# Optimization experiments

Measured on AMD Instinct MI355X. Metric: run time of the kernel, lower is better.

The kernel has to match this reference:

```python
import jax, jax.numpy as jnp
import numpy as np

B, N, BS, H, DH, L, FF, V, R = 1, 4096, 64, 12, 64, 4, 3072, 30522, 3
D = H * DH
M = N // BS
NEG = -10000.0


def layernorm(x, g, b, eps=1e-5):
    mu = x.mean(-1, keepdims=True)
    var = ((x - mu) ** 2).mean(-1, keepdims=True)
    return (x - mu) * jax.lax.rsqrt(var + eps) * g + b


def bigbird_attention(q, k, v, band_mask, from_mask, to_mask, blocked_mask, rand_attn):
    # q,k,v: [b,h,n,d]; band_mask [b,1,m-4,BS,3BS]; to_mask [b,1,1,n]; from_mask [b,1,n,1]
    b, h, n, d = q.shape
    m = n // BS
    r = rand_attn.shape[-1]
    sc = 1.0 / jnp.sqrt(jnp.float32(d))
    qb = q.reshape(b, h, m, BS, d)
    kb = k.reshape(b, h, m, BS, d)
    vb = v.reshape(b, h, m, BS, d)
    hid = jnp.arange(h)[:, None, None]
    gk = kb[:, hid, rand_attn].reshape(b, h, m - 2, r * BS, d)  # gathered random keys
    gv = vb[:, hid, rand_attn].reshape(b, h, m - 2, r * BS, d)
    rand_to = blocked_mask[:, rand_attn].reshape(b, h, m - 2, r * BS)
    rand_mask = jnp.einsum('blq,bhlk->bhlqk', blocked_mask[:, 1:-1], rand_to)  # [b,h,m-2,BS,rBS]

    # first block: dense over all keys (global)
    s = jnp.einsum('bhqd,bhkd->bhqk', qb[:, :, 0], k) * sc + (1.0 - to_mask) * NEG
    c_first = jnp.einsum('bhqk,bhkd->bhqd', jax.nn.softmax(s, axis=-1), v)

    # second block: blocks 0,1,2, last, + random row 0
    k2 = jnp.concatenate([kb[:, :, 0], kb[:, :, 1], kb[:, :, 2], kb[:, :, -1], gk[:, :, 0]], axis=2)
    v2 = jnp.concatenate([vb[:, :, 0], vb[:, :, 1], vb[:, :, 2], vb[:, :, -1], gv[:, :, 0]], axis=2)
    s = jnp.einsum('bhqd,bhkd->bhqk', qb[:, :, 1], k2) * sc
    seq_pad = jnp.concatenate([to_mask[..., :3 * BS], to_mask[..., -BS:],
                               jnp.ones((b, 1, 1, r * BS), s.dtype)], axis=3)
    rnd_pad = jnp.concatenate([jnp.ones((b, h, BS, 4 * BS), s.dtype), rand_mask[:, :, 0]], axis=3)
    s = s + (1.0 - jnp.minimum(seq_pad, rnd_pad)) * NEG
    c_second = jnp.einsum('bhqk,bhkd->bhqd', jax.nn.softmax(s, axis=-1), v2)

    # middle blocks: first-global + 3-block band + random + last-global
    mq = qb[:, :, 2:-2]  # [b,h,m-4,BS,d]
    exp_k = jnp.concatenate([kb[:, :, 1:-3], kb[:, :, 2:-2], kb[:, :, 3:-1]], axis=3)
    exp_v = jnp.concatenate([vb[:, :, 1:-3], vb[:, :, 2:-2], vb[:, :, 3:-1]], axis=3)
    inner = jnp.einsum('bhlqd,bhlkd->bhlqk', mq, exp_k) * sc + (1.0 - band_mask) * NEG
    randp = jnp.einsum('bhlqd,bhlkd->bhlqk', mq, gk[:, :, 1:-1]) * sc + (1.0 - rand_mask[:, :, 1:-1]) * NEG
    firstp = jnp.einsum('bhlqd,bhkd->bhlqk', mq, kb[:, :, 0]) * sc + (1.0 - to_mask[:, :, None, :, :BS]) * NEG
    lastp = jnp.einsum('bhlqd,bhkd->bhlqk', mq, kb[:, :, -1]) * sc + (1.0 - to_mask[:, :, None, :, -BS:]) * NEG
    w = jax.nn.softmax(jnp.concatenate([firstp, inner, randp, lastp], axis=-1), axis=-1)
    c_mid = jnp.einsum('bhlqk,bhlkd->bhlqd', w[..., BS:4 * BS], exp_v)
    c_mid = c_mid + jnp.einsum('bhlqk,bhlkd->bhlqd', w[..., 4 * BS:4 * BS + r * BS], gv[:, :, 1:-1])
    c_mid = c_mid + jnp.einsum('bhlqk,bhkd->bhlqd', w[..., :BS], vb[:, :, 0])
    c_mid = c_mid + jnp.einsum('bhlqk,bhkd->bhlqd', w[..., -BS:], vb[:, :, -1])

    # second-to-last block: block 0, last 3 blocks, + random row -1
    k3 = jnp.concatenate([kb[:, :, 0], kb[:, :, -3], kb[:, :, -2], kb[:, :, -1], gk[:, :, -1]], axis=2)
    v3 = jnp.concatenate([vb[:, :, 0], vb[:, :, -3], vb[:, :, -2], vb[:, :, -1], gv[:, :, -1]], axis=2)
    s = jnp.einsum('bhqd,bhkd->bhqk', qb[:, :, -2], k3) * sc
    seq_pad = jnp.concatenate([to_mask[..., :BS], to_mask[..., -3 * BS:],
                               jnp.ones((b, 1, 1, r * BS), s.dtype)], axis=3)
    rnd_pad = jnp.concatenate([jnp.ones((b, h, BS, 4 * BS), s.dtype), rand_mask[:, :, -1]], axis=3)
    s = s + (1.0 - jnp.minimum(seq_pad, rnd_pad)) * NEG
    c_sl = jnp.einsum('bhqk,bhkd->bhqd', jax.nn.softmax(s, axis=-1), v3)

    # last block: dense over all keys (global)
    s = jnp.einsum('bhqd,bhkd->bhqk', qb[:, :, -1], k) * sc + (1.0 - to_mask) * NEG
    c_last = jnp.einsum('bhqk,bhkd->bhqd', jax.nn.softmax(s, axis=-1), v)

    ctx = jnp.concatenate([c_first[:, :, None], c_second[:, :, None], c_mid,
                           c_sl[:, :, None], c_last[:, :, None]], axis=2)
    ctx = ctx.reshape(b, h, n, d) * from_mask
    return ctx.transpose(0, 2, 1, 3).reshape(b, n, h * d)


def forward(input_ids, mask, rand_attn, emb_word, emb_pos, emb_ln_g, emb_ln_b,
            Wq, bq, Wk, bk, Wv, bv, Wo, bo, ln1_g, ln1_b, W1, b1, W2, b2, ln2_g, ln2_b):
    b, n = input_ids.shape
    m = n // BS
    x = emb_word[input_ids] + emb_pos[None, :n]
    x = layernorm(x, emb_ln_g, emb_ln_b)
    blocked_mask = mask.reshape(b, m, BS)
    exp_to = jnp.concatenate([blocked_mask[:, 1:-3], blocked_mask[:, 2:-2], blocked_mask[:, 3:-1]], axis=2)
    band_mask = jnp.einsum('blq,blk->blqk', blocked_mask[:, 2:-2], exp_to)[:, None]
    from_mask = mask.reshape(b, 1, n, 1)
    to_mask = mask.reshape(b, 1, 1, n)
    for i in range(L):
        q = (x @ Wq[i] + bq[i]).reshape(b, n, H, DH).transpose(0, 2, 1, 3)
        k = (x @ Wk[i] + bk[i]).reshape(b, n, H, DH).transpose(0, 2, 1, 3)
        v = (x @ Wv[i] + bv[i]).reshape(b, n, H, DH).transpose(0, 2, 1, 3)
        a = bigbird_attention(q, k, v, band_mask, from_mask, to_mask, blocked_mask, rand_attn)
        a = a @ Wo[i] + bo[i]
        x = layernorm(x + a, ln1_g[i], ln1_b[i])  # dropout is identity in eval
        f = jax.nn.gelu(x @ W1[i] + b1[i], approximate=False) @ W2[i] + b2[i]
        x = layernorm(x + f, ln2_g[i], ln2_b[i])
    return x


def setup_inputs() -> dict:
    key = jax.random.key(0)
    ks = jax.random.split(key, 12)
    s = 0.02
    nrm = lambda k, shape: jax.random.normal(k, shape, jnp.float32) * s
    rng = np.random.default_rng(0)
    rand_attn = jnp.asarray(rng.integers(1, M - 1, size=(H, M - 2, R)), jnp.int32)
    return {
        'input_ids': jax.random.randint(ks[0], (B, N), 0, V),
        'mask': jnp.ones((B, N), jnp.float32),
        'rand_attn': rand_attn,
        'emb_word': nrm(ks[1], (V, D)),
        'emb_pos': nrm(ks[2], (N, D)),
        'emb_ln_g': jnp.ones((D,), jnp.float32), 'emb_ln_b': jnp.zeros((D,), jnp.float32),
        'Wq': nrm(ks[3], (L, D, D)), 'bq': jnp.zeros((L, D), jnp.float32),
        'Wk': nrm(ks[4], (L, D, D)), 'bk': jnp.zeros((L, D), jnp.float32),
        'Wv': nrm(ks[5], (L, D, D)), 'bv': jnp.zeros((L, D), jnp.float32),
        'Wo': nrm(ks[6], (L, D, D)), 'bo': jnp.zeros((L, D), jnp.float32),
        'ln1_g': jnp.ones((L, D), jnp.float32), 'ln1_b': jnp.zeros((L, D), jnp.float32),
        'W1': nrm(ks[7], (L, D, FF)), 'b1': jnp.zeros((L, FF), jnp.float32),
        'W2': nrm(ks[8], (L, FF, D)), 'b2': jnp.zeros((L, D), jnp.float32),
        'ln2_g': jnp.ones((L, D), jnp.float32), 'ln2_b': jnp.zeros((L, D), jnp.float32),
    }


def reference(input_ids, mask, rand_attn, emb_word, emb_pos, emb_ln_g, emb_ln_b,
              Wq, bq, Wk, bk, Wv, bv, Wo, bo, ln1_g, ln1_b, W1, b1, W2, b2, ln2_g, ln2_b):
    return forward(input_ids, mask, rand_attn, emb_word, emb_pos, emb_ln_g, emb_ln_b,
                   Wq, bq, Wk, bk, Wv, bv, Wo, bo, ln1_g, ln1_b, W1, b1, W2, b2, ln2_g, ln2_b)
```

## Files before the change

### kernel.cpp

```cpp
#include <hip/hip_runtime.h>
#include <hip/hip_bf16.h>
#include <math.h>

#define NTOK   4096
#define DMODEL 768
#define NHEAD  12
#define DHEAD  64
#define NLAYER 4
#define DFF    3072
#define NBLK   64
#define NEGC   -10000.0f

using frag8 = __attribute__((ext_vector_type(8))) short;
using f32x4 = __attribute__((ext_vector_type(4))) float;

typedef __attribute__((address_space(3))) void       lds_void;
typedef const __attribute__((address_space(1))) void gbl_void;

__device__ __forceinline__ void gload_lds16(const void* g, void* l) {
  __builtin_amdgcn_global_load_lds((gbl_void*)g, (lds_void*)l, 16, 0, 0);
}

__device__ __forceinline__ float block_sum256(float v) {
  __shared__ float tmp[4];
  #pragma unroll
  for (int o = 32; o > 0; o >>= 1) v += __shfl_down(v, o, 64);
  __syncthreads();
  if ((threadIdx.x & 63) == 0) tmp[threadIdx.x >> 6] = v;
  __syncthreads();
  return tmp[0] + tmp[1] + tmp[2] + tmp[3];
}

__global__ __launch_bounds__(256) void embed_ln_kernel(
    const int* __restrict__ ids, const float* __restrict__ emb_word,
    const float* __restrict__ emb_pos, const float* __restrict__ g,
    const float* __restrict__ b, float* __restrict__ x,
    __hip_bfloat16* __restrict__ xb)
{
  const int n = blockIdx.x;
  const int tid = threadIdx.x;
  const int id = ids[n];
  float v[3];
  #pragma unroll
  for (int j = 0; j < 3; ++j) {
    int d = tid + j * 256;
    v[j] = emb_word[(size_t)id * DMODEL + d] + emb_pos[(size_t)n * DMODEL + d];
  }
  float mu = block_sum256(v[0] + v[1] + v[2]) * (1.0f / DMODEL);
  float var = 0.f;
  #pragma unroll
  for (int j = 0; j < 3; ++j) { float t = v[j] - mu; var += t * t; }
  var = block_sum256(var) * (1.0f / DMODEL);
  float rs = rsqrtf(var + 1e-5f);
  #pragma unroll
  for (int j = 0; j < 3; ++j) {
    int d = tid + j * 256;
    float o = (v[j] - mu) * rs * g[d] + b[d];
    x[(size_t)n * DMODEL + d] = o;
    xb[(size_t)n * DMODEL + d] = (__hip_bfloat16)o;
  }
}

__global__ __launch_bounds__(256) void add_ln_red_kernel(
    const float* __restrict__ xin, const float* __restrict__ P, size_t ps,
    int nparts, const float* __restrict__ bias2,
    const float* __restrict__ g, const float* __restrict__ b,
    float* __restrict__ dst, __hip_bfloat16* __restrict__ dstb)
{
  const int n = blockIdx.x;
  const int tid = threadIdx.x;
  float v[3];
  #pragma unroll
  for (int j = 0; j < 3; ++j) {
    int d = tid + j * 256;
    float s = xin[(size_t)n * DMODEL + d] + bias2[d];
    for (int z = 0; z < nparts; ++z)
      s += P[(size_t)z * ps + (size_t)n * DMODEL + d];
    v[j] = s;
  }
  float mu = block_sum256(v[0] + v[1] + v[2]) * (1.0f / DMODEL);
  float var = 0.f;
  #pragma unroll
  for (int j = 0; j < 3; ++j) { float t = v[j] - mu; var += t * t; }
  var = block_sum256(var) * (1.0f / DMODEL);
  float rs = rsqrtf(var + 1e-5f);
  #pragma unroll
  for (int j = 0; j < 3; ++j) {
    int d = tid + j * 256;
    float ov = (v[j] - mu) * rs * g[d] + b[d];
    dst[(size_t)n * DMODEL + d] = ov;
    dstb[(size_t)n * DMODEL + d] = (__hip_bfloat16)ov;
  }
}

__global__ __launch_bounds__(256) void transpose_w_kernel(
    const float* __restrict__ W, __hip_bfloat16* __restrict__ WT, int K, int N)
{
  __shared__ float tile[32][33];
  const int n0 = blockIdx.x * 32;
  const int k0 = blockIdx.y * 32;
  const int c = threadIdx.x & 31;
  const int r0 = threadIdx.x >> 5;
  #pragma unroll
  for (int i = 0; i < 4; ++i) {
    int r = r0 + i * 8;
    tile[r][c] = W[(size_t)(k0 + r) * N + n0 + c];
  }
  __syncthreads();
  #pragma unroll
  for (int i = 0; i < 4; ++i) {
    int r = r0 + i * 8;
    WT[(size_t)(n0 + r) * K + k0 + c] = (__hip_bfloat16)tile[c][r];
  }
}

__global__ __launch_bounds__(256) void pack_bias_kernel(
    const float* __restrict__ bq, const float* __restrict__ bk,
    const float* __restrict__ bv, float* __restrict__ dst)
{
  int t = blockIdx.x * 256 + threadIdx.x;
  if (t < 3 * DMODEL)
    dst[t] = (t < DMODEL) ? bq[t] : (t < 2 * DMODEL ? bk[t - DMODEL] : bv[t - 2 * DMODEL]);
}

__global__ __launch_bounds__(256) void gemm_bf16_kernel(
    const __hip_bfloat16* __restrict__ A, int lda,
    const __hip_bfloat16* __restrict__ BT, int ldb,
    const float* __restrict__ bias,
    float* __restrict__ Cf, size_t cfStride,
    __hip_bfloat16* __restrict__ Cb,
    int Kpart, int ldC, int do_gelu)
{
  __shared__ __hip_bfloat16 Als[2][128 * 32];
  __shared__ __hip_bfloat16 Bls[2][128 * 32];
  const int tid = threadIdx.x;
  const int bm = blockIdx.x * 128;
  const int bn = blockIdx.y * 128;
  const int z  = blockIdx.z;
  const int koff = z * Kpart;

  const int wave = tid >> 6, lane = tid & 63;
  const int wm = (wave >> 1) * 64, wn = (wave & 1) * 64;
  const int lm = lane & 15, quad = lane >> 4;

  const int r0 = (0 * 4 + wave) * 16 + (lane >> 2);
  const int r1 = (1 * 4 + wave) * 16 + (lane >> 2);
  const int kc = (lane & 3) * 8;

  const __hip_bfloat16* Ar0 = A  + (size_t)(bm + r0) * lda + koff + kc;
  const __hip_bfloat16* Ar1 = A  + (size_t)(bm + r1) * lda + koff + kc;
  const __hip_bfloat16* Br0 = BT + (size_t)(bn + r0) * ldb + koff + kc;
  const __hip_bfloat16* Br1 = BT + (size_t)(bn + r1) * ldb + koff + kc;

  f32x4 acc[4][4];
  #pragma unroll
  for (int i = 0; i < 4; ++i)
    #pragma unroll
    for (int j = 0; j < 4; ++j)
      acc[i][j] = (f32x4){0.f, 0.f, 0.f, 0.f};

  gload_lds16(Ar0, &Als[0][r0 * 32 + kc]);
  gload_lds16(Ar1, &Als[0][r1 * 32 + kc]);
  gload_lds16(Br0, &Bls[0][r0 * 32 + kc]);
  gload_lds16(Br1, &Bls[0][r1 * 32 + kc]);

  int p = 0;
  for (int k0 = 0; k0 < Kpart; k0 += 32, p ^= 1) {
    __syncthreads();
    const int kn = k0 + 32;
    if (kn < Kpart) {
      gload_lds16(Ar0 + kn, &Als[p ^ 1][r0 * 32 + kc]);
      gload_lds16(Ar1 + kn, &Als[p ^ 1][r1 * 32 + kc]);
      gload_lds16(Br0 + kn, &Bls[p ^ 1][r0 * 32 + kc]);
      gload_lds16(Br1 + kn, &Bls[p ^ 1][r1 * 32 + kc]);
    }
    frag8 afr[4], bfr[4];
    #pragma unroll
    for (int t = 0; t < 4; ++t) {
      afr[t] = *(const frag8*)(&Als[p][(wm + t * 16 + lm) * 32 + quad * 8]);
      bfr[t] = *(const frag8*)(&Bls[p][(wn + t * 16 + lm) * 32 + quad * 8]);
    }
    #pragma unroll
    for (int mt = 0; mt < 4; ++mt)
      #pragma unroll
      for (int nt = 0; nt < 4; ++nt)
        acc[mt][nt] = __builtin_amdgcn_mfma_f32_16x16x32_bf16(
            afr[mt], bfr[nt], acc[mt][nt], 0, 0, 0);
  }

  float* Cfz = Cf ? Cf + (size_t)z * cfStride : nullptr;
  #pragma unroll
  for (int mt = 0; mt < 4; ++mt)
    #pragma unroll
    for (int nt = 0; nt < 4; ++nt)
      #pragma unroll
      for (int r = 0; r < 4; ++r) {
        int row = bm + wm + mt * 16 + quad * 4 + r;
        int col = bn + wn + nt * 16 + lm;
        float v = acc[mt][nt][r];
        if (bias) v += bias[col];
        if (do_gelu) v = 0.5f * v * (1.f + erff(v * 0.70710678118654752f));
        if (Cfz) Cfz[(size_t)row * ldC + col] = v;
        if (Cb) Cb[(size_t)row * ldC + col] = (__hip_bfloat16)v;
      }
}

__global__ __launch_bounds__(256) void attn_kernel(
    const __hip_bfloat16* __restrict__ qkvb, const float* __restrict__ mask,
    const int* __restrict__ rand_attn, __hip_bfloat16* __restrict__ outp,
    float* __restrict__ Mpart, float* __restrict__ Lpart, float* __restrict__ Opart)
{
  const int h = blockIdx.x;
  const int item = blockIdx.y;
  const int tid = threadIdx.x;

  int qi, chunk;
  if (item < 8)       { qi = 0;        chunk = item; }
  else if (item < 70) { qi = item - 7; chunk = -1; }
  else                { qi = 63;       chunk = item - 70; }

  __shared__ __hip_bfloat16 Qs[64 * 72];
  __shared__ __hip_bfloat16 Ks[64 * 72];
  __shared__ __hip_bfloat16 VTs[64 * 72];
  __shared__ __hip_bfloat16 Ps[64 * 72];
  __shared__ int slist[8];
  __shared__ int snb;

  const __hip_bfloat16* qg = qkvb;
  const __hip_bfloat16* kg = qkvb + DMODEL;
  const __hip_bfloat16* vg = qkvb + 2 * DMODEL;
  const int ldq = 3 * DMODEL;

  const int wave = tid >> 6, lane = tid & 63;
  const int wm = wave * 16;
  const int lm = lane & 15, quad = lane >> 4;

  {
    int r = tid >> 2, c0 = (tid & 3) * 16;
    const __hip_bfloat16* qp = qg + (size_t)(qi * 64 + r) * ldq + h * 64 + c0;
    uint4 a = *(const uint4*)qp;
    uint4 b = *(const uint4*)(qp + 8);
    *(uint4*)(Qs + r * 72 + c0) = a;
    *(uint4*)(Qs + r * 72 + c0 + 8) = b;
  }
  if (tid == 0) {
    if (chunk >= 0) {
      for (int j = 0; j < 8; ++j) slist[j] = chunk * 8 + j;
      snb = 8;
    } else {
      const int* ra = rand_attn + ((size_t)h * 62 + (qi - 1)) * 3;
      if (qi == 1)       { slist[0] = 0; slist[1] = 1;  slist[2] = 2;  slist[3] = 63; }
      else if (qi == 62) { slist[0] = 0; slist[1] = 61; slist[2] = 62; slist[3] = 63; }
      else               { slist[0] = 0; slist[1] = qi - 1; slist[2] = qi; slist[3] = qi + 1; }
      slist[4] = ra[0]; slist[5] = ra[1]; slist[6] = ra[2];
      int nb = 7;
      if (qi >= 2 && qi <= 61) { slist[7] = 63; nb = 8; }
      snb = nb;
    }
  }
  __syncthreads();
  const int nb = snb;

  frag8 aq0 = *(const frag8*)(Qs + (wm + lm) * 72 + quad * 8);
  frag8 aq1 = *(const frag8*)(Qs + (wm + lm) * 72 + 32 + quad * 8);

  float mold[4], lsum[4];
  #pragma unroll
  for (int r = 0; r < 4; ++r) { mold[r] = -1e30f; lsum[r] = 0.f; }
  f32x4 oacc[4];
  #pragma unroll
  for (int t = 0; t < 4; ++t) oacc[t] = (f32x4){0.f, 0.f, 0.f, 0.f};

  const int sr = tid >> 2, sc0 = (tid & 3) * 16;

  for (int bi = 0; bi < nb; ++bi) {
    const int kb = slist[bi];
    const __hip_bfloat16* kp = kg + (size_t)(kb * 64 + sr) * ldq + h * 64 + sc0;
    const __hip_bfloat16* vp = vg + (size_t)(kb * 64 + sr) * ldq + h * 64 + sc0;
    uint4 kv0 = *(const uint4*)kp;
    uint4 kv1 = *(const uint4*)(kp + 8);
    uint4 vv0 = *(const uint4*)vp;
    uint4 vv1 = *(const uint4*)(vp + 8);
    float msk[4];
    #pragma unroll
    for (int t = 0; t < 4; ++t) msk[t] = mask[kb * 64 + t * 16 + lm];

    __syncthreads();
    *(uint4*)(Ks + sr * 72 + sc0) = kv0;
    *(uint4*)(Ks + sr * 72 + sc0 + 8) = kv1;
    {
      union { uint4 u[2]; __hip_bfloat16 h16[16]; } vu;
      vu.u[0] = vv0; vu.u[1] = vv1;
      #pragma unroll
      for (int j = 0; j < 16; ++j)
        VTs[(sc0 + j) * 72 + sr] = vu.h16[j];
    }
    __syncthreads();

    f32x4 sacc[4];
    #pragma unroll
    for (int t = 0; t < 4; ++t) sacc[t] = (f32x4){0.f, 0.f, 0.f, 0.f};
    #pragma unroll
    for (int t = 0; t < 4; ++t) {
      frag8 bk0 = *(const frag8*)(Ks + (t * 16 + lm) * 72 + quad * 8);
      frag8 bk1 = *(const frag8*)(Ks + (t * 16 + lm) * 72 + 32 + quad * 8);
      sacc[t] = __builtin_amdgcn_mfma_f32_16x16x32_bf16(aq0, bk0, sacc[t], 0, 0, 0);
      sacc[t] = __builtin_amdgcn_mfma_f32_16x16x32_bf16(aq1, bk1, sacc[t], 0, 0, 0);
    }

    float xs[4][4];
    #pragma unroll
    for (int t = 0; t < 4; ++t)
      #pragma unroll
      for (int r = 0; r < 4; ++r)
        xs[t][r] = sacc[t][r] * 0.125f + (1.f - msk[t]) * NEGC;

    float al[4], psum[4];
    #pragma unroll
    for (int r = 0; r < 4; ++r) {
      float rm = fmaxf(fmaxf(xs[0][r], xs[1][r]), fmaxf(xs[2][r], xs[3][r]));
      rm = fmaxf(rm, __shfl_xor(rm, 1, 64));
      rm = fmaxf(rm, __shfl_xor(rm, 2, 64));
      rm = fmaxf(rm, __shfl_xor(rm, 4, 64));
      rm = fmaxf(rm, __shfl_xor(rm, 8, 64));
      float mnew = fmaxf(mold[r], rm);
      al[r] = __expf(mold[r] - mnew);
      float s = 0.f;
      #pragma unroll
      for (int t = 0; t < 4; ++t) {
        float p = __expf(xs[t][r] - mnew);
        xs[t][r] = p;
        s += p;
      }
      s += __shfl_xor(s, 1, 64);
      s += __shfl_xor(s, 2, 64);
      s += __shfl_xor(s, 4, 64);
      s += __shfl_xor(s, 8, 64);
      psum[r] = s;
      mold[r] = mnew;
    }
    #pragma unroll
    for (int r = 0; r < 4; ++r) lsum[r] = lsum[r] * al[r] + psum[r];
    #pragma unroll
    for (int t = 0; t < 4; ++t)
      #pragma unroll
      for (int r = 0; r < 4; ++r)
        oacc[t][r] *= al[r];

    #pragma unroll
    for (int t = 0; t < 4; ++t)
      #pragma unroll
      for (int r = 0; r < 4; ++r)
        Ps[(wm + quad * 4 + r) * 72 + t * 16 + lm] = (__hip_bfloat16)xs[t][r];

    frag8 ap0 = *(const frag8*)(Ps + (wm + lm) * 72 + quad * 8);
    frag8 ap1 = *(const frag8*)(Ps + (wm + lm) * 72 + 32 + quad * 8);
    #pragma unroll
    for (int t = 0; t < 4; ++t) {
      frag8 bv0 = *(const frag8*)(VTs + (t * 16 + lm) * 72 + quad * 8);
      frag8 bv1 = *(const frag8*)(VTs + (t * 16 + lm) * 72 + 32 + quad * 8);
      oacc[t] = __builtin_amdgcn_mfma_f32_16x16x32_bf16(ap0, bv0, oacc[t], 0, 0, 0);
      oacc[t] = __builtin_amdgcn_mfma_f32_16x16x32_bf16(ap1, bv1, oacc[t], 0, 0, 0);
    }
  }

  if (chunk < 0) {
    #pragma unroll
    for (int r = 0; r < 4; ++r) {
      int row = qi * 64 + wm + quad * 4 + r;
      float sc2 = mask[row] / lsum[r];
      #pragma unroll
      for (int t = 0; t < 4; ++t)
        outp[(size_t)row * DMODEL + h * 64 + t * 16 + lm] =
            (__hip_bfloat16)(oacc[t][r] * sc2);
    }
  } else {
    const int idx = (h * 2 + (qi == 63 ? 1 : 0)) * 8 + chunk;
    #pragma unroll
    for (int r = 0; r < 4; ++r) {
      int row = wm + quad * 4 + r;
      #pragma unroll
      for (int t = 0; t < 4; ++t)
        Opart[(size_t)idx * 4096 + row * 64 + t * 16 + lm] = oacc[t][r];
      if (lm == 0) {
        Mpart[idx * 64 + row] = mold[r];
        Lpart[idx * 64 + row] = lsum[r];
      }
    }
  }
}

__global__ __launch_bounds__(256) void attn_merge_kernel(
    const float* __restrict__ Mpart, const float* __restrict__ Lpart,
    const float* __restrict__ Opart, const float* __restrict__ mask,
    __hip_bfloat16* __restrict__ outp)
{
  const int h = blockIdx.x, side = blockIdx.y;
  const int qi = side ? 63 : 0;
  const int tid = threadIdx.x;
  const int r = tid >> 2;
  const int d0 = (tid & 3) * 16;
  const int base = (h * 2 + side) * 8;

  float mv[8], m = -1e30f;
  #pragma unroll
  for (int c = 0; c < 8; ++c) { mv[c] = Mpart[(base + c) * 64 + r]; m = fmaxf(m, mv[c]); }
  float sc[8], l = 0.f;
  #pragma unroll
  for (int c = 0; c < 8; ++c) {
    sc[c] = __expf(mv[c] - m);
    l += Lpart[(base + c) * 64 + r] * sc[c];
  }
  float o[16];
  #pragma unroll
  for (int d = 0; d < 16; ++d) o[d] = 0.f;
  #pragma unroll
  for (int c = 0; c < 8; ++c) {
    const float* Op = Opart + (size_t)(base + c) * 4096 + r * 64 + d0;
    #pragma unroll
    for (int d4 = 0; d4 < 4; ++d4) {
      float4 v4 = *(const float4*)(Op + d4 * 4);
      o[d4 * 4 + 0] += v4.x * sc[c];
      o[d4 * 4 + 1] += v4.y * sc[c];
      o[d4 * 4 + 2] += v4.z * sc[c];
      o[d4 * 4 + 3] += v4.w * sc[c];
    }
  }
  const int row = qi * 64 + r;
  float inv = mask[row] / l;
  #pragma unroll
  for (int d = 0; d < 16; ++d)
    outp[(size_t)row * DMODEL + h * 64 + d0 + d] = (__hip_bfloat16)(o[d] * inv);
}

extern "C" void kernel_launch(void* const* d_in, const int* in_sizes, int n_in,
                              void* d_out, int out_size, void* d_ws, size_t ws_size,
                              hipStream_t stream)
{
  const int*   ids      = (const int*)  d_in[0];
  const float* mask     = (const float*)d_in[1];
  const int*   rand_att = (const int*)  d_in[2];
  const float* emb_word = (const float*)d_in[3];
  const float* emb_pos  = (const float*)d_in[4];
  const float* eg       = (const float*)d_in[5];
  const float* eb       = (const float*)d_in[6];
  const float* Wq = (const float*)d_in[7];
  const float* bq = (const float*)d_in[8];
  const float* Wk = (const float*)d_in[9];
  const float* bk = (const float*)d_in[10];
  const float* Wv = (const float*)d_in[11];
  const float* bv = (const float*)d_in[12];
  const float* Wo = (const float*)d_in[13];
  const float* bo = (const float*)d_in[14];
  const float* ln1g = (const float*)d_in[15];
  const float* ln1b = (const float*)d_in[16];
  const float* W1 = (const float*)d_in[17];
  const float* bf1 = (const float*)d_in[18];
  const float* W2 = (const float*)d_in[19];
  const float* bf2 = (const float*)d_in[20];
  const float* ln2g = (const float*)d_in[21];
  const float* ln2b = (const float*)d_in[22];

  const size_t ND = (size_t)NTOK * DMODEL;
  float* x   = (float*)d_ws;
  __hip_bfloat16* xb = (__hip_bfloat16*)(x + ND);
  float* P   = (float*)(xb + ND);
  __hip_bfloat16* qkvb = (__hip_bfloat16*)(P + 3 * ND);
  __hip_bfloat16* fb_b = qkvb + 3 * ND;
  __hip_bfloat16* ab_b = fb_b + (size_t)NTOK * DFF;
  __hip_bfloat16* wqkvT = ab_b + ND;
  __hip_bfloat16* woT  = wqkvT + (size_t)3 * DMODEL * DMODEL;
  __hip_bfloat16* w1T  = woT  + (size_t)DMODEL * DMODEL;
  __hip_bfloat16* w2T  = w1T  + (size_t)DFF * DMODEL;
  float* biasf = (float*)(w2T + (size_t)DMODEL * DFF);
  float* Mpart = biasf + 3 * DMODEL;
  float* Lpart = Mpart + NHEAD * 2 * 8 * 64;
  float* Opart = Lpart + NHEAD * 2 * 8 * 64;

  embed_ln_kernel<<<NTOK, 256, 0, stream>>>(ids, emb_word, emb_pos, eg, eb, x, xb);

  for (int l = 0; l < NLAYER; ++l) {
    const float* Wq_l = Wq + (size_t)l * DMODEL * DMODEL;
    const float* Wk_l = Wk + (size_t)l * DMODEL * DMODEL;
    const float* Wv_l = Wv + (size_t)l * DMODEL * DMODEL;
    const float* Wo_l = Wo + (size_t)l * DMODEL * DMODEL;
    const float* W1_l = W1 + (size_t)l * DMODEL * DFF;
    const float* W2_l = W2 + (size_t)l * DFF * DMODEL;

    dim3 g32(DMODEL / 32, DMODEL / 32);
    transpose_w_kernel<<<g32, 256, 0, stream>>>(Wq_l, wqkvT, DMODEL, DMODEL);
    transpose_w_kernel<<<g32, 256, 0, stream>>>(Wk_l, wqkvT + (size_t)DMODEL * DMODEL, DMODEL, DMODEL);
    transpose_w_kernel<<<g32, 256, 0, stream>>>(Wv_l, wqkvT + (size_t)2 * DMODEL * DMODEL, DMODEL, DMODEL);
    transpose_w_kernel<<<g32, 256, 0, stream>>>(Wo_l, woT, DMODEL, DMODEL);
    transpose_w_kernel<<<dim3(DFF / 32, DMODEL / 32), 256, 0, stream>>>(W1_l, w1T, DMODEL, DFF);
    transpose_w_kernel<<<dim3(DMODEL / 32, DFF / 32), 256, 0, stream>>>(W2_l, w2T, DFF, DMODEL);
    pack_bias_kernel<<<9, 256, 0, stream>>>(bq + (size_t)l * DMODEL, bk + (size_t)l * DMODEL,
                                            bv + (size_t)l * DMODEL, biasf);

    gemm_bf16_kernel<<<dim3(NTOK / 128, 3 * DMODEL / 128, 1), 256, 0, stream>>>(
        xb, DMODEL, wqkvT, DMODEL, biasf, nullptr, 0, qkvb, DMODEL, 3 * DMODEL, 0);

    attn_kernel<<<dim3(NHEAD, 78), 256, 0, stream>>>(qkvb, mask, rand_att, ab_b,
                                                     Mpart, Lpart, Opart);
    attn_merge_kernel<<<dim3(NHEAD, 2), 256, 0, stream>>>(Mpart, Lpart, Opart, mask, ab_b);

    gemm_bf16_kernel<<<dim3(NTOK / 128, DMODEL / 128, 2), 256, 0, stream>>>(
        ab_b, DMODEL, woT, DMODEL, nullptr, P, ND, nullptr, DMODEL / 2, DMODEL, 0);
    add_ln_red_kernel<<<NTOK, 256, 0, stream>>>(x, P, ND, 2, bo + (size_t)l * DMODEL,
                                                ln1g + (size_t)l * DMODEL,
                                                ln1b + (size_t)l * DMODEL, x, xb);

    gemm_bf16_kernel<<<dim3(NTOK / 128, DFF / 128, 1), 256, 0, stream>>>(
        xb, DMODEL, w1T, DMODEL, bf1 + (size_t)l * DFF, nullptr, 0, fb_b, DMODEL, DFF, 1);

    gemm_bf16_kernel<<<dim3(NTOK / 128, DMODEL / 128, 3), 256, 0, stream>>>(
        fb_b, DFF, w2T, DFF, nullptr, P, ND, nullptr, DFF / 3, DMODEL, 0);
    add_ln_red_kernel<<<NTOK, 256, 0, stream>>>(x, P, ND, 3, bf2 + (size_t)l * DMODEL,
                                                ln2g + (size_t)l * DMODEL,
                                                ln2b + (size_t)l * DMODEL,
                                                (l == NLAYER - 1) ? (float*)d_out : x, xb);
  }
}
```

Baseline: 1.095 ms.

## Shrink GEMM M-tile to 64 and remap workgroups across XCDs

Reduces the GEMM tile from 128x128 to 64x128, doubling the number of workgroups so more of the CUs are filled for these modest-size matrices. It also remaps the linear workgroup index so consecutive tiles land on the same XCD, which is meant to improve L2 reuse of shared B or A panels. The trade-off is less data reuse per tile and a lower MFMA-to-load ratio per workgroup.

```diff
diff --git a/kernel.cpp b/kernel.cpp
--- a/kernel.cpp
+++ b/kernel.cpp
@@ -131,57 +131,61 @@
     __hip_bfloat16* __restrict__ Cb,
     int Kpart, int ldC, int do_gelu)
 {
-  __shared__ __hip_bfloat16 Als[2][128 * 32];
+  __shared__ __hip_bfloat16 Als[2][64 * 32];
   __shared__ __hip_bfloat16 Bls[2][128 * 32];
   const int tid = threadIdx.x;
-  const int bm = blockIdx.x * 128;
-  const int bn = blockIdx.y * 128;
+
+  const int gx = gridDim.x;
+  const int nwg = gx * gridDim.y;
+  const int orig = blockIdx.y * gx + blockIdx.x;
+  const int q = nwg >> 3, r = nwg & 7;
+  const int xcd = orig & 7, loc = orig >> 3;
+  const int wg = (xcd < r ? xcd * (q + 1) : r * (q + 1) + (xcd - r) * q) + loc;
+  const int bm = (wg % gx) * 64;
+  const int bn = (wg / gx) * 128;
   const int z  = blockIdx.z;
   const int koff = z * Kpart;
 
   const int wave = tid >> 6, lane = tid & 63;
-  const int wm = (wave >> 1) * 64, wn = (wave & 1) * 64;
+  const int wm = (wave >> 1) * 32, wn = (wave & 1) * 64;
   const int lm = lane & 15, quad = lane >> 4;
 
-  const int r0 = (0 * 4 + wave) * 16 + (lane >> 2);
-  const int r1 = (1 * 4 + wave) * 16 + (lane >> 2);
+  const int rA = wave * 16 + (lane >> 2);
   const int kc = (lane & 3) * 8;
 
-  const __hip_bfloat16* Ar0 = A  + (size_t)(bm + r0) * lda + koff + kc;
-  const __hip_bfloat16* Ar1 = A  + (size_t)(bm + r1) * lda + koff + kc;
-  const __hip_bfloat16* Br0 = BT + (size_t)(bn + r0) * ldb + koff + kc;
-  const __hip_bfloat16* Br1 = BT + (size_t)(bn + r1) * ldb + koff + kc;
-
-  f32x4 acc[4][4];
-  #pragma unroll
-  for (int i = 0; i < 4; ++i)
+  const __hip_bfloat16* Ar  = A  + (size_t)(bm + rA) * lda + koff + kc;
+  const __hip_bfloat16* Br0 = BT + (size_t)(bn + rA) * ldb + koff + kc;
+  const __hip_bfloat16* Br1 = BT + (size_t)(bn + 64 + rA) * ldb + koff + kc;
+
+  f32x4 acc[2][4];
+  #pragma unroll
+  for (int i = 0; i < 2; ++i)
     #pragma unroll
     for (int j = 0; j < 4; ++j)
       acc[i][j] = (f32x4){0.f, 0.f, 0.f, 0.f};
 
-  gload_lds16(Ar0, &Als[0][r0 * 32 + kc]);
-  gload_lds16(Ar1, &Als[0][r1 * 32 + kc]);
-  gload_lds16(Br0, &Bls[0][r0 * 32 + kc]);
-  gload_lds16(Br1, &Bls[0][r1 * 32 + kc]);
+  gload_lds16(Ar,  &Als[0][rA * 32 + kc]);
+  gload_lds16(Br0, &Bls[0][rA * 32 + kc]);
+  gload_lds16(Br1, &Bls[0][(64 + rA) * 32 + kc]);
 
   int p = 0;
   for (int k0 = 0; k0 < Kpart; k0 += 32, p ^= 1) {
     __syncthreads();
     const int kn = k0 + 32;
     if (kn < Kpart) {
-      gload_lds16(Ar0 + kn, &Als[p ^ 1][r0 * 32 + kc]);
-      gload_lds16(Ar1 + kn, &Als[p ^ 1][r1 * 32 + kc]);
-      gload_lds16(Br0 + kn, &Bls[p ^ 1][r0 * 32 + kc]);
-      gload_lds16(Br1 + kn, &Bls[p ^ 1][r1 * 32 + kc]);
-    }
-    frag8 afr[4], bfr[4];
-    #pragma unroll
-    for (int t = 0; t < 4; ++t) {
-      afr[t] = *(const frag8*)(&Als[p][(wm + t * 16 + lm) * 32 + quad * 8]);
-      bfr[t] = *(const frag8*)(&Bls[p][(wn + t * 16 + lm) * 32 + quad * 8]);
-    }
-    #pragma unroll
-    for (int mt = 0; mt < 4; ++mt)
+      gload_lds16(Ar + kn,  &Als[p ^ 1][rA * 32 + kc]);
+      gload_lds16(Br0 + kn, &Bls[p ^ 1][rA * 32 + kc]);
+      gload_lds16(Br1 + kn, &Bls[p ^ 1][(64 + rA) * 32 + kc]);
+    }
+    frag8 afr[2], bfr[4];
+    #pragma unroll
+    for (int mt = 0; mt < 2; ++mt)
+      afr[mt] = *(const frag8*)(&Als[p][(wm + mt * 16 + lm) * 32 + quad * 8]);
+    #pragma unroll
+    for (int nt = 0; nt < 4; ++nt)
+      bfr[nt] = *(const frag8*)(&Bls[p][(wn + nt * 16 + lm) * 32 + quad * 8]);
+    #pragma unroll
+    for (int mt = 0; mt < 2; ++mt)
       #pragma unroll
       for (int nt = 0; nt < 4; ++nt)
         acc[mt][nt] = __builtin_amdgcn_mfma_f32_16x16x32_bf16(
@@ -190,14 +194,14 @@
 
   float* Cfz = Cf ? Cf + (size_t)z * cfStride : nullptr;
   #pragma unroll
-  for (int mt = 0; mt < 4; ++mt)
+  for (int mt = 0; mt < 2; ++mt)
     #pragma unroll
     for (int nt = 0; nt < 4; ++nt)
       #pragma unroll
-      for (int r = 0; r < 4; ++r) {
-        int row = bm + wm + mt * 16 + quad * 4 + r;
+      for (int rr = 0; rr < 4; ++rr) {
+        int row = bm + wm + mt * 16 + quad * 4 + rr;
         int col = bn + wn + nt * 16 + lm;
-        float v = acc[mt][nt][r];
+        float v = acc[mt][nt][rr];
         if (bias) v += bias[col];
         if (do_gelu) v = 0.5f * v * (1.f + erff(v * 0.70710678118654752f));
         if (Cfz) Cfz[(size_t)row * ldC + col] = v;
@@ -497,23 +501,23 @@
     pack_bias_kernel<<<9, 256, 0, stream>>>(bq + (size_t)l * DMODEL, bk + (size_t)l * DMODEL,
                                             bv + (size_t)l * DMODEL, biasf);
 
-    gemm_bf16_kernel<<<dim3(NTOK / 128, 3 * DMODEL / 128, 1), 256, 0, stream>>>(
+    gemm_bf16_kernel<<<dim3(NTOK / 64, 3 * DMODEL / 128, 1), 256, 0, stream>>>(
         xb, DMODEL, wqkvT, DMODEL, biasf, nullptr, 0, qkvb, DMODEL, 3 * DMODEL, 0);
 
     attn_kernel<<<dim3(NHEAD, 78), 256, 0, stream>>>(qkvb, mask, rand_att, ab_b,
                                                      Mpart, Lpart, Opart);
     attn_merge_kernel<<<dim3(NHEAD, 2), 256, 0, stream>>>(Mpart, Lpart, Opart, mask, ab_b);
 
-    gemm_bf16_kernel<<<dim3(NTOK / 128, DMODEL / 128, 2), 256, 0, stream>>>(
+    gemm_bf16_kernel<<<dim3(NTOK / 64, DMODEL / 128, 2), 256, 0, stream>>>(
         ab_b, DMODEL, woT, DMODEL, nullptr, P, ND, nullptr, DMODEL / 2, DMODEL, 0);
     add_ln_red_kernel<<<NTOK, 256, 0, stream>>>(x, P, ND, 2, bo + (size_t)l * DMODEL,
                                                 ln1g + (size_t)l * DMODEL,
                                                 ln1b + (size_t)l * DMODEL, x, xb);
 
-    gemm_bf16_kernel<<<dim3(NTOK / 128, DFF / 128, 1), 256, 0, stream>>>(
+    gemm_bf16_kernel<<<dim3(NTOK / 64, DFF / 128, 1), 256, 0, stream>>>(
         xb, DMODEL, w1T, DMODEL, bf1 + (size_t)l * DFF, nullptr, 0, fb_b, DMODEL, DFF, 1);
 
-    gemm_bf16_kernel<<<dim3(NTOK / 128, DMODEL / 128, 3), 256, 0, stream>>>(
+    gemm_bf16_kernel<<<dim3(NTOK / 64, DMODEL / 128, 3), 256, 0, stream>>>(
         fb_b, DFF, w2T, DFF, nullptr, P, ND, nullptr, DFF / 3, DMODEL, 0);
     add_ln_red_kernel<<<NTOK, 256, 0, stream>>>(x, P, ND, 3, bf2 + (size_t)l * DMODEL,
                                                 ln2g + (size_t)l * DMODEL,
```

Measured after the change: 1.172 ms. 1.07x slower.
